# Kernel tuning notes

Hardware: AMD Instinct MI355X
Metric: run time of the kernel (lower is better)

The kernel has to match this reference:

```python
import jax, jax.numpy as jnp
import numpy as np

N = 100000      # num_nodes
E = 6400000     # num edges
D = 128         # embedding_dim
R = 8           # num_roles
ALPHA = 0.15
ITERS = 10

def setup_inputs() -> dict:
    key = jax.random.key(0)
    k1, k2, k3, k4, k5 = jax.random.split(key, 5)
    edge_index = jax.random.randint(k1, (2, E), 0, N)
    batch_nodes = jax.random.randint(k2, (N,), 0, N)
    importance_emb = jax.random.normal(k3, (N, D), dtype=jnp.float32)
    resizer_W = jax.random.normal(k4, (D, 2), dtype=jnp.float32) * (1.0 / np.sqrt(D))
    resizer_b = jnp.zeros((2,), dtype=jnp.float32)
    # xavier_uniform for behavior_matrix [R, 4]
    limit = np.sqrt(6.0 / (R + 4))
    behavior_matrix = jax.random.uniform(k5, (R, 4), minval=-limit, maxval=limit, dtype=jnp.float32)
    return {
        'edge_index': edge_index,
        'batch_nodes': batch_nodes,
        'importance_emb': importance_emb,
        'resizer_W': resizer_W,
        'resizer_b': resizer_b,
        'behavior_matrix': behavior_matrix,
    }

def reference(edge_index, batch_nodes, importance_emb, resizer_W, resizer_b, behavior_matrix):
    src, dst = edge_index[0], edge_index[1]
    num_edges = src.shape[0]
    # out-degrees via segment_sum (== bincount)
    out_deg = jax.ops.segment_sum(jnp.ones((num_edges,), jnp.float32), src, num_segments=N)
    inv_deg_src = 1.0 / jnp.maximum(out_deg, 1.0)[src]  # [E], clamp(min=1)

    # approximate_pagerank: 10 iterations of gather -> scale -> scatter_add
    def body(pr, _):
        contrib = (1.0 - ALPHA) * pr[src] * inv_deg_src
        new_pr = jax.ops.segment_sum(contrib, dst, num_segments=N) + ALPHA / N
        return new_pr, None
    pr0 = jnp.full((N,), 1.0 / N, dtype=jnp.float32)
    pagerank, _ = jax.lax.scan(body, pr0, None, length=ITERS)

    # resizer: single Linear(D, 2)
    emb2 = importance_emb @ resizer_W + resizer_b  # [B, 2]

    # X = [deg[batch], pagerank[batch], emb2] -> [B, 4]
    X = jnp.concatenate([out_deg[batch_nodes][:, None],
                         pagerank[batch_nodes][:, None],
                         emb2], axis=1)

    # lstsq(H.T, X.T): A = H.T is [4, R], underdetermined -> minimum-norm
    # solution Z = A^T (A A^T)^{-1} X^T ; W = Z^T  -> [B, R]
    A = behavior_matrix.T                      # [4, R]
    G = A @ A.T                                # [4, 4]
    W = (A.T @ jnp.linalg.solve(G, X.T)).T     # [B, R]

    # F.normalize(W, p=2, dim=1)
    norm = jnp.linalg.norm(W, axis=1, keepdims=True)
    roles = W / jnp.maximum(norm, 1e-12)
    return roles
```

## Files before the change

### kernel.cpp

```cpp
#include <hip/hip_runtime.h>
#include <math.h>

#define N_NODES 100000
#define N_EDGES 6400000
#define DIM     128
#define NROLES  8
#define ALPHA   0.15f
#define PR_ITERS 10

#define BUCKET_SHIFT 9
#define BUCKET_SIZE  512
#define NBUCKET      196
#define NB2          392
#define NBLK_BIN     256
#define CHUNK        25000
#define SEG          8

__global__ void k_prep_M(const float* __restrict__ H, float* __restrict__ Mout) {
    if (threadIdx.x != 0 || blockIdx.x != 0) return;
    double G[4][4];
    for (int i = 0; i < 4; ++i)
        for (int j = 0; j < 4; ++j) {
            double s = 0.0;
            for (int r = 0; r < NROLES; ++r)
                s += (double)H[r * 4 + i] * (double)H[r * 4 + j];
            G[i][j] = s;
        }
    double aug[4][8];
    for (int i = 0; i < 4; ++i)
        for (int j = 0; j < 4; ++j) {
            aug[i][j] = G[i][j];
            aug[i][j + 4] = (i == j) ? 1.0 : 0.0;
        }
    for (int c = 0; c < 4; ++c) {
        int p = c; double best = fabs(aug[c][c]);
        for (int r = c + 1; r < 4; ++r) {
            double v = fabs(aug[r][c]);
            if (v > best) { best = v; p = r; }
        }
        if (p != c)
            for (int j = 0; j < 8; ++j) {
                double t = aug[c][j]; aug[c][j] = aug[p][j]; aug[p][j] = t;
            }
        double piv = aug[c][c];
        for (int j = 0; j < 8; ++j) aug[c][j] /= piv;
        for (int r = 0; r < 4; ++r) {
            if (r == c) continue;
            double f = aug[r][c];
            for (int j = 0; j < 8; ++j) aug[r][j] -= f * aug[c][j];
        }
    }
    for (int r = 0; r < NROLES; ++r)
        for (int k = 0; k < 4; ++k) {
            double s = 0.0;
            for (int j = 0; j < 4; ++j)
                s += (double)H[r * 4 + j] * aug[j][k + 4];
            Mout[r * 4 + k] = (float)s;
        }
}

__global__ __launch_bounds__(256)
void k_hist(const int* __restrict__ src, const int* __restrict__ dst,
            unsigned* __restrict__ counts) {
    __shared__ unsigned h[NB2];
    for (int i = threadIdx.x; i < NB2; i += 256) h[i] = 0;
    __syncthreads();
    int beg = blockIdx.x * CHUNK;
    int t = threadIdx.x;
    int mainEnd = beg + 24576;
    for (int e = beg + t * 4; e < mainEnd; e += 1024) {
        int4 s4 = *(const int4*)(src + e);
        int4 d4 = *(const int4*)(dst + e);
        atomicAdd(&h[((unsigned)d4.x) >> BUCKET_SHIFT], 1u);
        atomicAdd(&h[((unsigned)d4.y) >> BUCKET_SHIFT], 1u);
        atomicAdd(&h[((unsigned)d4.z) >> BUCKET_SHIFT], 1u);
        atomicAdd(&h[((unsigned)d4.w) >> BUCKET_SHIFT], 1u);
        atomicAdd(&h[NBUCKET + (((unsigned)s4.x) >> BUCKET_SHIFT)], 1u);
        atomicAdd(&h[NBUCKET + (((unsigned)s4.y) >> BUCKET_SHIFT)], 1u);
        atomicAdd(&h[NBUCKET + (((unsigned)s4.z) >> BUCKET_SHIFT)], 1u);
        atomicAdd(&h[NBUCKET + (((unsigned)s4.w) >> BUCKET_SHIFT)], 1u);
    }
    for (int e = mainEnd + t; e < beg + CHUNK; e += 256) {
        atomicAdd(&h[((unsigned)dst[e]) >> BUCKET_SHIFT], 1u);
        atomicAdd(&h[NBUCKET + (((unsigned)src[e]) >> BUCKET_SHIFT)], 1u);
    }
    __syncthreads();
    for (int i = threadIdx.x; i < NB2; i += 256)
        counts[blockIdx.x * NB2 + i] = h[i];
}

__global__ __launch_bounds__(256)
void k_scanA(const unsigned* __restrict__ counts, unsigned* __restrict__ offs,
             unsigned* __restrict__ btot) {
    int bucket = blockIdx.x, t = threadIdx.x, lane = t & 63, wv = t >> 6;
    unsigned v = counts[t * NB2 + bucket], x = v;
    #pragma unroll
    for (int o = 1; o < 64; o <<= 1) {
        unsigned y = __shfl_up(x, o);
        if (lane >= o) x += y;
    }
    __shared__ unsigned wsum[4];
    if (lane == 63) wsum[wv] = x;
    __syncthreads();
    unsigned carry = 0;
    for (int w = 0; w < wv; ++w) carry += wsum[w];
    x += carry;
    offs[t * NB2 + bucket] = x - v;
    if (t == 255) btot[bucket] = x;
}

__global__ __launch_bounds__(256)
void k_scanB(const unsigned* __restrict__ btot, unsigned* __restrict__ bases) {
    int half = blockIdx.x;
    int t = threadIdx.x, lane = t & 63, wv = t >> 6;
    unsigned v = (t < NBUCKET) ? btot[half * NBUCKET + t] : 0u, x = v;
    #pragma unroll
    for (int o = 1; o < 64; o <<= 1) {
        unsigned y = __shfl_up(x, o);
        if (lane >= o) x += y;
    }
    __shared__ unsigned wsum[4];
    if (lane == 63) wsum[wv] = x;
    __syncthreads();
    unsigned carry = 0;
    for (int w = 0; w < wv; ++w) carry += wsum[w];
    x += carry;
    if (t <= NBUCKET) bases[half * 256 + t] = x - v;
}

__global__ __launch_bounds__(256)
void k_place(const int* __restrict__ src, const int* __restrict__ dst,
             const unsigned* __restrict__ offs, const unsigned* __restrict__ bases,
             unsigned* __restrict__ rec, unsigned short* __restrict__ recs) {
    __shared__ unsigned cD[NBUCKET];
    __shared__ unsigned cS[NBUCKET];
    for (int i = threadIdx.x; i < NBUCKET; i += 256) {
        cD[i] = bases[i]       + offs[blockIdx.x * NB2 + i];
        cS[i] = bases[256 + i] + offs[blockIdx.x * NB2 + NBUCKET + i];
    }
    __syncthreads();
    int beg = blockIdx.x * CHUNK;
    int t = threadIdx.x;
    int mainEnd = beg + 24576;
    for (int e = beg + t * 4; e < mainEnd; e += 1024) {
        int4 s4 = *(const int4*)(src + e);
        int4 d4 = *(const int4*)(dst + e);
        #pragma unroll
        for (int k = 0; k < 4; ++k) {
            unsigned s = (unsigned)((&s4.x)[k]);
            unsigned d = (unsigned)((&d4.x)[k]);
            unsigned pos = atomicAdd(&cD[d >> BUCKET_SHIFT], 1u);
            rec[pos] = ((d & (BUCKET_SIZE - 1)) << 17) | s;
            unsigned pos2 = atomicAdd(&cS[s >> BUCKET_SHIFT], 1u);
            recs[pos2] = (unsigned short)(s & (BUCKET_SIZE - 1));
        }
    }
    for (int e = mainEnd + t; e < beg + CHUNK; e += 256) {
        unsigned s = (unsigned)src[e];
        unsigned d = (unsigned)dst[e];
        unsigned pos = atomicAdd(&cD[d >> BUCKET_SHIFT], 1u);
        rec[pos] = ((d & (BUCKET_SIZE - 1)) << 17) | s;
        unsigned pos2 = atomicAdd(&cS[s >> BUCKET_SHIFT], 1u);
        recs[pos2] = (unsigned short)(s & (BUCKET_SIZE - 1));
    }
}

__global__ __launch_bounds__(256)
void k_count_init(const unsigned short* __restrict__ recs,
                  const unsigned* __restrict__ bases,
                  float* __restrict__ deg, float* __restrict__ s,
                  float* __restrict__ val0) {
    __shared__ unsigned cnt[BUCKET_SIZE];
    int t = threadIdx.x;
    cnt[t] = 0; cnt[t + 256] = 0;
    __syncthreads();
    int b = blockIdx.x;
    unsigned st = bases[256 + b], en = bases[256 + b + 1];
    unsigned a = (st + 7u) & ~7u;
    if (a > en) a = en;
    for (unsigned i = st + t; i < a; i += 256)
        atomicAdd(&cnt[recs[i]], 1u);
    unsigned mainN = (en - a) & ~2047u;
    const uint4* rp = (const uint4*)(recs + a);
    for (unsigned i = t; i * 8u < mainN; i += 256) {
        uint4 r = rp[i];
        atomicAdd(&cnt[r.x & 0xFFFFu], 1u); atomicAdd(&cnt[r.x >> 16], 1u);
        atomicAdd(&cnt[r.y & 0xFFFFu], 1u); atomicAdd(&cnt[r.y >> 16], 1u);
        atomicAdd(&cnt[r.z & 0xFFFFu], 1u); atomicAdd(&cnt[r.z >> 16], 1u);
        atomicAdd(&cnt[r.w & 0xFFFFu], 1u); atomicAdd(&cnt[r.w >> 16], 1u);
    }
    for (unsigned i = a + mainN + t; i < en; i += 256)
        atomicAdd(&cnt[recs[i]], 1u);
    __syncthreads();
    #pragma unroll
    for (int k = 0; k < 2; ++k) {
        int v = b * BUCKET_SIZE + t + k * 256;
        if (v < N_NODES) {
            float d = (float)cnt[t + k * 256];
            float sv = (1.0f - ALPHA) / fmaxf(d, 1.0f);
            deg[v] = d;
            s[v] = sv;
            val0[v] = sv * (1.0f / (float)N_NODES);
        }
    }
}

__global__ __launch_bounds__(256)
void k_iter2(const unsigned* __restrict__ rec, const unsigned* __restrict__ bases,
             const float* __restrict__ val, float* __restrict__ partial) {
    __shared__ float acc[BUCKET_SIZE];
    int t = threadIdx.x;
    acc[t] = 0.0f;
    acc[t + 256] = 0.0f;
    __syncthreads();
    int b   = blockIdx.x >> 3;
    int seg = blockIdx.x & 7;
    unsigned st = bases[b], en = bases[b + 1], n = en - st;
    unsigned s0 = st + (unsigned)(((unsigned long long)n * (unsigned)seg) >> 3);
    unsigned s1 = st + (unsigned)(((unsigned long long)n * (unsigned)(seg + 1)) >> 3);
    unsigned a0 = (s0 + 3u) & ~3u;
    if (a0 > s1) a0 = s1;
    for (unsigned i = s0 + t; i < a0; i += 256) {
        unsigned r = rec[i];
        atomicAdd(&acc[r >> 17], val[r & 0x1FFFFu]);
    }
    unsigned nv = (s1 - a0) >> 2;
    const uint4* rp = (const uint4*)(rec + a0);
    for (unsigned i = t; i < nv; i += 256) {
        uint4 r = rp[i];
        float v0 = val[r.x & 0x1FFFFu];
        float v1 = val[r.y & 0x1FFFFu];
        float v2 = val[r.z & 0x1FFFFu];
        float v3 = val[r.w & 0x1FFFFu];
        atomicAdd(&acc[r.x >> 17], v0);
        atomicAdd(&acc[r.y >> 17], v1);
        atomicAdd(&acc[r.z >> 17], v2);
        atomicAdd(&acc[r.w >> 17], v3);
    }
    for (unsigned i = a0 + nv * 4u + t; i < s1; i += 256) {
        unsigned r = rec[i];
        atomicAdd(&acc[r >> 17], val[r & 0x1FFFFu]);
    }
    __syncthreads();
    float* p = partial + ((unsigned)blockIdx.x << 9);
    p[t] = acc[t];
    p[t + 256] = acc[t + 256];
}

__global__ __launch_bounds__(256)
void k_reduce(const float* __restrict__ partial, const float* __restrict__ s,
              float* __restrict__ pr, float* __restrict__ valn) {
    int v = blockIdx.x * 256 + threadIdx.x;
    if (v >= N_NODES) return;
    int b = v >> BUCKET_SHIFT, local = v & (BUCKET_SIZE - 1);
    const float* p = partial + ((unsigned)(b * SEG) << 9) + local;
    float sum = 0.0f;
    #pragma unroll
    for (int k = 0; k < SEG; ++k) sum += p[k << 9];
    float pv = sum + ALPHA / (float)N_NODES;
    pr[v] = pv;
    valn[v] = pv * s[v];
}

__global__ __launch_bounds__(256)
void k_final(const float* __restrict__ emb, const float* __restrict__ rW,
             const float* __restrict__ rb, const int* __restrict__ batch,
             const float* __restrict__ deg, const float* __restrict__ pr,
             const float* __restrict__ M, float* __restrict__ out) {
    int wid  = (blockIdx.x * blockDim.x + threadIdx.x) >> 6;
    int lane = threadIdx.x & 63;
    if (wid >= N_NODES) return;

    const float* row = emb + (size_t)wid * DIM;
    float e0 = row[lane];
    float e1 = row[lane + 64];
    float2 w0 = ((const float2*)rW)[lane];
    float2 w1 = ((const float2*)rW)[lane + 64];
    float a0 = e0 * w0.x + e1 * w1.x;
    float a1 = e0 * w0.y + e1 * w1.y;
    #pragma unroll
    for (int off = 32; off; off >>= 1) {
        a0 += __shfl_xor(a0, off);
        a1 += __shfl_xor(a1, off);
    }

    int bn = batch[wid];
    float x0 = deg[bn];
    float x1 = pr[bn];
    float x2 = a0 + rb[0];
    float x3 = a1 + rb[1];

    float wr = 0.0f;
    if (lane < NROLES) {
        const float* m = M + lane * 4;
        wr = m[0] * x0 + m[1] * x1 + m[2] * x2 + m[3] * x3;
    }
    float sq = wr * wr;
    #pragma unroll
    for (int off = 4; off; off >>= 1) sq += __shfl_xor(sq, off);
    float inv = 1.0f / fmaxf(sqrtf(sq), 1e-12f);
    if (lane < NROLES) out[(size_t)wid * NROLES + lane] = wr * inv;
}

extern "C" void kernel_launch(void* const* d_in, const int* in_sizes, int n_in,
                              void* d_out, int out_size, void* d_ws, size_t ws_size,
                              hipStream_t stream) {
    const int*   edge  = (const int*)d_in[0];
    const int*   src   = edge;
    const int*   dst   = edge + N_EDGES;
    const int*   batch = (const int*)d_in[1];
    const float* emb   = (const float*)d_in[2];
    const float* rW    = (const float*)d_in[3];
    const float* rb    = (const float*)d_in[4];
    const float* H     = (const float*)d_in[5];
    float*       out   = (float*)d_out;

    float*    deg    = (float*)d_ws;
    float*    s      = deg   + 100352;
    float*    pr     = s     + 100352;
    float*    valA   = pr    + 100352;
    float*    valB   = valA  + 100352;
    float*    M      = valB  + 100352;
    unsigned* counts = (unsigned*)(M + 32);
    unsigned* offs   = counts + NBLK_BIN * NB2;
    unsigned* btot   = offs   + NBLK_BIN * NB2;
    unsigned* bases  = btot   + 512;
    unsigned* rec    = bases  + 512;
    unsigned short* recs = (unsigned short*)(rec + N_EDGES);
    float*    partial = (float*)(recs + N_EDGES);

    k_prep_M<<<1, 1, 0, stream>>>(H, M);

    k_hist <<<NBLK_BIN, 256, 0, stream>>>(src, dst, counts);
    k_scanA<<<NB2,      256, 0, stream>>>(counts, offs, btot);
    k_scanB<<<2,        256, 0, stream>>>(btot, bases);
    k_place<<<NBLK_BIN, 256, 0, stream>>>(src, dst, offs, bases, rec, recs);
    k_count_init<<<NBUCKET, 256, 0, stream>>>(recs, bases, deg, s, valA);

    float* vcur = valA;
    float* vnxt = valB;
    for (int it = 0; it < PR_ITERS; ++it) {
        k_iter2 <<<NBUCKET * SEG, 256, 0, stream>>>(rec, bases, vcur, partial);
        k_reduce<<<(N_NODES + 255) / 256, 256, 0, stream>>>(partial, s, pr, vnxt);
        float* t = vcur; vcur = vnxt; vnxt = t;
    }

    const int FG = (N_NODES + 3) / 4;
    k_final<<<FG, 256, 0, stream>>>(emb, rW, rb, batch, deg, pr, M, out);
}
```

Before: 541.6 us.

## Sort edge records by source within each bucket and unroll gather loop

```diff
diff --git a/kernel.cpp b/kernel.cpp
--- a/kernel.cpp
+++ b/kernel.cpp
@@ -15,6 +15,7 @@
 #define NBLK_BIN     256
 #define CHUNK        25000
 #define SEG          8
+#define SBINS        1792
 
 __global__ void k_prep_M(const float* __restrict__ H, float* __restrict__ Mout) {
     if (threadIdx.x != 0 || blockIdx.x != 0) return;
@@ -206,6 +207,44 @@
 }
 
 __global__ __launch_bounds__(256)
+void k_sort(const unsigned* __restrict__ rec, const unsigned* __restrict__ bases,
+            unsigned* __restrict__ rec2) {
+    __shared__ unsigned hist[SBINS];
+    __shared__ unsigned wsum[4];
+    int t = threadIdx.x, lane = t & 63, wv = t >> 6;
+    for (int i = t; i < SBINS; i += 256) hist[i] = 0;
+    __syncthreads();
+    int b = blockIdx.x;
+    unsigned st = bases[b], en = bases[b + 1];
+    for (unsigned i = st + t; i < en; i += 256)
+        atomicAdd(&hist[(rec[i] & 0x1FFFFu) >> 6], 1u);
+    __syncthreads();
+    unsigned loc[7], sum = 0;
+    #pragma unroll
+    for (int k = 0; k < 7; ++k) { loc[k] = hist[t * 7 + k]; sum += loc[k]; }
+    unsigned x = sum;
+    #pragma unroll
+    for (int o = 1; o < 64; o <<= 1) {
+        unsigned y = __shfl_up(x, o);
+        if (lane >= o) x += y;
+    }
+    if (lane == 63) wsum[wv] = x;
+    __syncthreads();
+    unsigned carry = 0;
+    for (int w = 0; w < wv; ++w) carry += wsum[w];
+    unsigned base = carry + x - sum;
+    __syncthreads();
+    #pragma unroll
+    for (int k = 0; k < 7; ++k) { hist[t * 7 + k] = base; base += loc[k]; }
+    __syncthreads();
+    for (unsigned i = st + t; i < en; i += 256) {
+        unsigned r = rec[i];
+        unsigned pos = atomicAdd(&hist[(r & 0x1FFFFu) >> 6], 1u);
+        rec2[st + pos] = r;
+    }
+}
+
+__global__ __launch_bounds__(256)
 void k_iter2(const unsigned* __restrict__ rec, const unsigned* __restrict__ bases,
              const float* __restrict__ val, float* __restrict__ partial) {
     __shared__ float acc[BUCKET_SIZE];
@@ -220,24 +259,35 @@
     unsigned s1 = st + (unsigned)(((unsigned long long)n * (unsigned)(seg + 1)) >> 3);
     unsigned a0 = (s0 + 3u) & ~3u;
     if (a0 > s1) a0 = s1;
+    unsigned nq = (s1 - a0) >> 2;
+    unsigned nh = nq >> 1;
+    const uint4* rp = (const uint4*)(rec + a0);
+    unsigned tail0 = a0 + 8u * nh;
     for (unsigned i = s0 + t; i < a0; i += 256) {
         unsigned r = rec[i];
         atomicAdd(&acc[r >> 17], val[r & 0x1FFFFu]);
     }
-    unsigned nv = (s1 - a0) >> 2;
-    const uint4* rp = (const uint4*)(rec + a0);
-    for (unsigned i = t; i < nv; i += 256) {
-        uint4 r = rp[i];
-        float v0 = val[r.x & 0x1FFFFu];
-        float v1 = val[r.y & 0x1FFFFu];
-        float v2 = val[r.z & 0x1FFFFu];
-        float v3 = val[r.w & 0x1FFFFu];
-        atomicAdd(&acc[r.x >> 17], v0);
-        atomicAdd(&acc[r.y >> 17], v1);
-        atomicAdd(&acc[r.z >> 17], v2);
-        atomicAdd(&acc[r.w >> 17], v3);
-    }
-    for (unsigned i = a0 + nv * 4u + t; i < s1; i += 256) {
+    for (unsigned i = t; i < nh; i += 256) {
+        uint4 ra = rp[i];
+        uint4 rb2 = rp[i + nh];
+        float v0 = val[ra.x & 0x1FFFFu];
+        float v1 = val[ra.y & 0x1FFFFu];
+        float v2 = val[ra.z & 0x1FFFFu];
+        float v3 = val[ra.w & 0x1FFFFu];
+        float v4 = val[rb2.x & 0x1FFFFu];
+        float v5 = val[rb2.y & 0x1FFFFu];
+        float v6 = val[rb2.z & 0x1FFFFu];
+        float v7 = val[rb2.w & 0x1FFFFu];
+        atomicAdd(&acc[ra.x >> 17], v0);
+        atomicAdd(&acc[ra.y >> 17], v1);
+        atomicAdd(&acc[ra.z >> 17], v2);
+        atomicAdd(&acc[ra.w >> 17], v3);
+        atomicAdd(&acc[rb2.x >> 17], v4);
+        atomicAdd(&acc[rb2.y >> 17], v5);
+        atomicAdd(&acc[rb2.z >> 17], v6);
+        atomicAdd(&acc[rb2.w >> 17], v7);
+    }
+    for (unsigned i = tail0 + t; i < s1; i += 256) {
         unsigned r = rec[i];
         atomicAdd(&acc[r >> 17], val[r & 0x1FFFFu]);
     }
@@ -326,8 +376,9 @@
     unsigned* btot   = offs   + NBLK_BIN * NB2;
     unsigned* bases  = btot   + 512;
     unsigned* rec    = bases  + 512;
-    unsigned short* recs = (unsigned short*)(rec + N_EDGES);
-    float*    partial = (float*)(recs + N_EDGES);
+    unsigned* rec2   = rec    + N_EDGES;
+    unsigned short* recs = (unsigned short*)rec2;
+    float*    partial = (float*)(rec2 + N_EDGES);
 
     k_prep_M<<<1, 1, 0, stream>>>(H, M);
 
@@ -336,11 +387,12 @@
     k_scanB<<<2,        256, 0, stream>>>(btot, bases);
     k_place<<<NBLK_BIN, 256, 0, stream>>>(src, dst, offs, bases, rec, recs);
     k_count_init<<<NBUCKET, 256, 0, stream>>>(recs, bases, deg, s, valA);
+    k_sort <<<NBUCKET, 256, 0, stream>>>(rec, bases, rec2);
 
     float* vcur = valA;
     float* vnxt = valB;
     for (int it = 0; it < PR_ITERS; ++it) {
-        k_iter2 <<<NBUCKET * SEG, 256, 0, stream>>>(rec, bases, vcur, partial);
+        k_iter2 <<<NBUCKET * SEG, 256, 0, stream>>>(rec2, bases, vcur, partial);
         k_reduce<<<(N_NODES + 255) / 256, 256, 0, stream>>>(partial, s, pr, vnxt);
         float* t = vcur; vcur = vnxt; vnxt = t;
     }
```

Measured after the change: 634.7 us. 17.2% more time.
